# Performance work log

Hardware: AMD Instinct MI355X
Metric: run time of the kernel (lower is better)

The kernel has to match this reference:

```python
import jax, jax.numpy as jnp
import numpy as np

B, N, DIN, D, PHI, RHO, L = 4096, 10, 32, 128, 256, 128, 3
EPS = 1e-5


def setup_inputs() -> dict:
    key = jax.random.key(0)
    ks = jax.random.split(key, 24)
    def p(k, shape):
        return jax.random.normal(k, shape, jnp.float32) * 0.05
    return {
        "A": jax.random.normal(ks[0], (B, N, N), jnp.float32),
        "X": jax.random.normal(ks[1], (B, N, DIN), jnp.float32),
        "home_mask": jax.random.randint(ks[2], (B, N), 0, 2).astype(jnp.int32),
        "We1": p(ks[3], (DIN, D)), "be1": p(ks[4], (D,)),
        "We2": p(ks[5], (D, D)), "be2": p(ks[6], (D,)),
        "rgcn_w": p(ks[7], (L, 2, D, D)),      # per-relation weights
        "rgcn_root": p(ks[8], (L, D, D)),       # root (self) weight
        "rgcn_b": p(ks[9], (L, D)),
        "l1w": p(ks[10], (L, D, D)), "l1b": p(ks[11], (L, D)),
        "l2w": p(ks[12], (L, D, D)), "l2b": p(ks[13], (L, D)),
        "ln_g": jnp.ones((D,), jnp.float32), "ln_b": jnp.zeros((D,), jnp.float32),
        "p1w": p(ks[14], (D, PHI)), "p1b": p(ks[15], (PHI,)),
        "p2w": p(ks[16], (PHI, PHI)), "p2b": p(ks[17], (PHI,)),
        "r1w": p(ks[18], (PHI, RHO)), "r1b": p(ks[19], (RHO,)),
        "r2w": p(ks[20], (RHO, 1)), "r2b": p(ks[21], (1,)),
    }


def _layernorm(x, g, b):
    mu = x.mean(-1, keepdims=True)
    var = ((x - mu) ** 2).mean(-1, keepdims=True)
    return (x - mu) / jnp.sqrt(var + EPS) * g + b


def reference(A, X, home_mask, We1, be1, We2, be2, rgcn_w, rgcn_root, rgcn_b,
              l1w, l1b, l2w, l2b, ln_g, ln_b, p1w, p1b, p2w, p2b,
              r1w, r1b, r2w, r2b):
    BN = B * N
    hm = home_mask.astype(jnp.float32)
    am = 1.0 - hm
    # embedders (dropout layers are identity in eval)
    H = jax.nn.relu(X @ We1 + be1)
    H = (H @ We2 + be2).reshape(BN, D)
    # A ~ randn is nonzero everywhere -> edge list = all (b,i,j) pairs,
    # in the same row-major order torch.nonzero produces.
    bidx = jnp.repeat(jnp.arange(BN), N)          # b*N+i for each edge (row)
    row = bidx
    col = (jnp.repeat(jnp.arange(B), N * N) * N + jnp.tile(jnp.arange(N), BN))
    ew = A.reshape(-1)                             # edge weight
    aw = jnp.abs(ew)
    m1 = (ew > 0).astype(jnp.float32)              # relation 1 mask
    m0 = 1.0 - m1                                  # relation 0 mask
    agg = jnp.zeros_like(H)
    for l in range(L):
        H = H + agg
        # RGCNConv (mean aggregation per relation + root + bias)
        xj = H[row]                                # [E, D] gather of sources
        s0 = jax.ops.segment_sum(xj * m0[:, None], col, num_segments=BN)
        s1 = jax.ops.segment_sum(xj * m1[:, None], col, num_segments=BN)
        c0 = jax.ops.segment_sum(m0, col, num_segments=BN)
        c1 = jax.ops.segment_sum(m1, col, num_segments=BN)
        mean0 = s0 / jnp.maximum(c0, 1.0)[:, None]
        mean1 = s1 / jnp.maximum(c1, 1.0)[:, None]
        H2 = mean0 @ rgcn_w[l, 0] + mean1 @ rgcn_w[l, 1] + H @ rgcn_root[l] + rgcn_b[l]
        # outer gather-scale-scatter
        msg = H2[col] * aw[:, None]                # [E, D]
        agg = jax.ops.segment_sum(msg, row, num_segments=BN)
        agg = jax.nn.relu(_layernorm(agg, ln_g, ln_b))
        # Linear -> ReLU -> (Dropout=id) -> Linear
        agg = jax.nn.relu(agg @ l1w[l] + l1b[l])
        agg = agg @ l2w[l] + l2b[l]
    H = (H + agg).reshape(B, N, D)
    # DeepSet phi (dropout = identity)
    phi = jax.nn.relu(H @ p1w + p1b)
    phi = jax.nn.relu(phi @ p2w + p2b)             # [B, N, PHI]
    hs = (phi * hm[..., None]).sum(axis=1)
    aws = (phi * am[..., None]).sum(axis=1)
    def rho(s):
        return (jax.nn.relu(s @ r1w + r1b) @ r2w + r2b)[..., 0]
    return 0.5 + 0.5 * jnp.tanh(rho(hs) - rho(aws))
```

## Files before the change

### kernel.cpp

```cpp
#include <hip/hip_runtime.h>
#include <math.h>

#define B_    4096
#define N_    10
#define DIN_  32
#define D_    128
#define PHI_  256
#define RHO_  128
#define L_    3
#define EPS_  1e-5f

__device__ __forceinline__ short f2hs(float f) {
    union { _Float16 h; short s; } u;
    u.h = (_Float16)f;
    return u.s;
}
__device__ __forceinline__ float hs2f(short s) {
    union { _Float16 h; short s; } u;
    u.s = s;
    return (float)u.h;
}

typedef short   s16x8 __attribute__((ext_vector_type(8)));
typedef _Float16 h16x8 __attribute__((ext_vector_type(8)));
typedef float   f32x4 __attribute__((ext_vector_type(4)));
typedef float   v2f   __attribute__((ext_vector_type(2)));

__device__ __forceinline__ h16x8 ld8h(const short* p) {
    union { s16x8 s; h16x8 h; } u;
    u.s = *(const s16x8*)p;
    return u.h;
}

__device__ __forceinline__ v2f splat2(float s) { v2f r; r.x = s; r.y = s; return r; }
__device__ __forceinline__ v2f fma2(v2f a, v2f b, v2f c) { return __builtin_elementwise_fma(a, b, c); }

#define WS_WE1 0
#define WS_WE2 4096
#define WS_RGW 20480
#define WS_RGR 118784
#define WS_L1  167936
#define WS_L2  217088
#define WS_P1  266240
#define WS_P2  299008
#define WS_R1  364544

__global__ __launch_bounds__(64)
void prep_weights(const float* __restrict__ We1, const float* __restrict__ We2,
                  const float* __restrict__ rgw, const float* __restrict__ rgr,
                  const float* __restrict__ l1w, const float* __restrict__ l2w,
                  const float* __restrict__ p1w, const float* __restrict__ p2w,
                  const float* __restrict__ r1w, short* __restrict__ ws)
{
    int bi = blockIdx.x, l = threadIdx.x;
    const float* src; int KS, Nw, dstOff, tt;
    if      (bi <   8) { src = We1; KS = 1; Nw = 128; dstOff = WS_WE1; tt = bi; }
    else if (bi <  40) { src = We2; KS = 4; Nw = 128; dstOff = WS_WE2; tt = bi - 8; }
    else if (bi < 232) { int m = (bi - 40) >> 5;  src = rgw + m * 16384; KS = 4; Nw = 128; dstOff = WS_RGW + m * 16384; tt = (bi - 40)  & 31; }
    else if (bi < 328) { int m = (bi - 232) >> 5; src = rgr + m * 16384; KS = 4; Nw = 128; dstOff = WS_RGR + m * 16384; tt = (bi - 232) & 31; }
    else if (bi < 424) { int m = (bi - 328) >> 5; src = l1w + m * 16384; KS = 4; Nw = 128; dstOff = WS_L1  + m * 16384; tt = (bi - 328) & 31; }
    else if (bi < 520) { int m = (bi - 424) >> 5; src = l2w + m * 16384; KS = 4; Nw = 128; dstOff = WS_L2  + m * 16384; tt = (bi - 424) & 31; }
    else if (bi < 584) { src = p1w; KS = 4; Nw = 256; dstOff = WS_P1; tt = bi - 520; }
    else if (bi < 712) { src = p2w; KS = 8; Nw = 256; dstOff = WS_P2; tt = bi - 584; }
    else               { src = r1w; KS = 8; Nw = 128; dstOff = WS_R1; tt = bi - 712; }
    int nt = tt / KS, ks = tt - nt * KS;
    int kbase = ks * 32 + (l >> 4) * 8;
    int col   = nt * 16 + (l & 15);
    union { short s[8]; int4 v; } u;
#pragma unroll
    for (int j = 0; j < 8; ++j)
        u.s[j] = f2hs(src[(size_t)(kbase + j) * Nw + col]);
    *(int4*)(ws + dstOff + ((size_t)tt * 64 + l) * 8) = u.v;
}


template<int NT>
__device__ __forceinline__ void initC(f32x4* acc, const float* __restrict__ bias, int c16) {
#pragma unroll
    for (int nt = 0; nt < NT; ++nt) {
        float bv = bias[nt * 16 + c16];
        acc[nt] = (f32x4){bv, bv, bv, bv};
    }
}

template<int KS, int NT>
__device__ __forceinline__ void mm_a16(const short* __restrict__ Wf, const short* __restrict__ Ab,
                                       int ldA, int mrow, int q, int l, f32x4* acc) {
#pragma unroll
    for (int ks = 0; ks < KS; ++ks) {
        h16x8 a = ld8h(Ab + mrow * ldA + ks * 32 + q * 8);
#pragma unroll
        for (int nt = 0; nt < NT; ++nt) {
            h16x8 bv = ld8h(Wf + ((size_t)(nt * KS + ks) * 64 + l) * 8);
            acc[nt] = __builtin_amdgcn_mfma_f32_16x16x32_f16(a, bv, acc[nt], 0, 0, 0);
        }
    }
}

template<int KS, int NT>
__device__ __forceinline__ void mm_a32(const short* __restrict__ Wf, const float* __restrict__ Af,
                                       int ldA, int mrow, int q, int l, f32x4* acc) {
#pragma unroll
    for (int ks = 0; ks < KS; ++ks) {
        const float* p = Af + mrow * ldA + ks * 32 + q * 8;
        f32x4 x0 = *(const f32x4*)p;
        f32x4 x1 = *(const f32x4*)(p + 4);
        h16x8 a;
        a[0] = (_Float16)x0[0]; a[1] = (_Float16)x0[1]; a[2] = (_Float16)x0[2]; a[3] = (_Float16)x0[3];
        a[4] = (_Float16)x1[0]; a[5] = (_Float16)x1[1]; a[6] = (_Float16)x1[2]; a[7] = (_Float16)x1[3];
#pragma unroll
        for (int nt = 0; nt < NT; ++nt) {
            h16x8 bv = ld8h(Wf + ((size_t)(nt * KS + ks) * 64 + l) * 8);
            acc[nt] = __builtin_amdgcn_mfma_f32_16x16x32_f16(a, bv, acc[nt], 0, 0, 0);
        }
    }
}

template<int KS>
__device__ __forceinline__ void mm8p_a16(const short* __restrict__ Wf,
                                         const short* __restrict__ Ab, int ldA,
                                         int mrow, int q, int l, f32x4* acc)
{
    const short* ap = Ab + mrow * ldA + q * 8;
    const short* wp = Wf + l * 8;
    h16x8 acur = ld8h(ap);
    h16x8 bcur[8], bnxt[8];
#pragma unroll
    for (int nt = 0; nt < 8; ++nt) bcur[nt] = ld8h(wp + (size_t)nt * KS * 512);
#pragma unroll
    for (int ks = 0; ks < KS; ++ks) {
        h16x8 anxt = acur;
#pragma unroll
        for (int nt = 0; nt < 8; ++nt) bnxt[nt] = bcur[nt];
        if (ks + 1 < KS) {
            anxt = ld8h(ap + (ks + 1) * 32);
#pragma unroll
            for (int nt = 0; nt < 8; ++nt)
                bnxt[nt] = ld8h(wp + (size_t)(nt * KS + ks + 1) * 512);
        }
#pragma unroll
        for (int nt = 0; nt < 8; ++nt)
            acc[nt] = __builtin_amdgcn_mfma_f32_16x16x32_f16(acur, bcur[nt], acc[nt], 0, 0, 0);
        acur = anxt;
#pragma unroll
        for (int nt = 0; nt < 8; ++nt) bcur[nt] = bnxt[nt];
    }
}

template<int KS>
__device__ __forceinline__ void mm8p_a32(const short* __restrict__ Wf,
                                         const float* __restrict__ Af, int ldA,
                                         int mrow, int q, int l, f32x4* acc)
{
    const float* ap = Af + mrow * ldA + q * 8;
    const short* wp = Wf + l * 8;
    auto cvt = [&](int ks) {
        f32x4 x0 = *(const f32x4*)(ap + ks * 32);
        f32x4 x1 = *(const f32x4*)(ap + ks * 32 + 4);
        h16x8 a;
        a[0] = (_Float16)x0[0]; a[1] = (_Float16)x0[1]; a[2] = (_Float16)x0[2]; a[3] = (_Float16)x0[3];
        a[4] = (_Float16)x1[0]; a[5] = (_Float16)x1[1]; a[6] = (_Float16)x1[2]; a[7] = (_Float16)x1[3];
        return a;
    };
    h16x8 acur = cvt(0);
    h16x8 bcur[8], bnxt[8];
#pragma unroll
    for (int nt = 0; nt < 8; ++nt) bcur[nt] = ld8h(wp + (size_t)nt * KS * 512);
#pragma unroll
    for (int ks = 0; ks < KS; ++ks) {
        h16x8 anxt = acur;
#pragma unroll
        for (int nt = 0; nt < 8; ++nt) bnxt[nt] = bcur[nt];
        if (ks + 1 < KS) {
            anxt = cvt(ks + 1);
#pragma unroll
            for (int nt = 0; nt < 8; ++nt)
                bnxt[nt] = ld8h(wp + (size_t)(nt * KS + ks + 1) * 512);
        }
#pragma unroll
        for (int nt = 0; nt < 8; ++nt)
            acc[nt] = __builtin_amdgcn_mfma_f32_16x16x32_f16(acur, bcur[nt], acc[nt], 0, 0, 0);
        acur = anxt;
#pragma unroll
        for (int nt = 0; nt < 8; ++nt) bcur[nt] = bnxt[nt];
    }
}

template<int NT, bool RELU>
__device__ __forceinline__ void storeC16(const f32x4* acc, short* __restrict__ dst,
                                         int ldD, int q, int c16) {
#pragma unroll
    for (int nt = 0; nt < NT; ++nt) {
#pragma unroll
        for (int i = 0; i < 4; ++i) {
            int r = q * 4 + i;
            if (r < 10) {
                float v = acc[nt][i];
                if (RELU) v = fmaxf(v, 0.f);
                dst[r * ldD + nt * 16 + c16] = f2hs(v);
            }
        }
    }
}

#define HLD 132
#define MLD 136
#define GLD 264

__global__ __launch_bounds__(64, 2)
void gcn_main(const float* __restrict__ A, const float* __restrict__ X,
              const int* __restrict__ home_mask,
              const float* __restrict__ be1, const float* __restrict__ be2,
              const float* __restrict__ rgcn_b,
              const float* __restrict__ l1b, const float* __restrict__ l2b,
              const float* __restrict__ ln_g, const float* __restrict__ ln_b,
              const float* __restrict__ p1b, const float* __restrict__ p2b,
              const float* __restrict__ r1b, const float* __restrict__ r2w,
              const short* __restrict__ ws, float* __restrict__ out)
{
    const int b   = blockIdx.x;
    const int l   = threadIdx.x;
    const int q   = l >> 4;
    const int c16 = l & 15;
    const int mrow = (c16 < 10) ? c16 : 9;

    __shared__ __align__(16) float HfS[N_ * HLD];
    __shared__ __align__(16) short Me0S[N_ * MLD];
    __shared__ __align__(16) short Me1S[N_ * MLD];
    __shared__ __align__(16) short GbS[N_ * GLD];
    __shared__ __align__(16) short RhoS[2 * 256];
    __shared__ float AabsS[100], M1S[100];
    __shared__ float invc0S[N_], invc1S[N_];
    __shared__ float hmfS[16], awfS[16];

    {
        const float* Ab = A + (size_t)b * 100;
#pragma unroll
        for (int e = l; e < 100; e += 64) {
            float a = Ab[e];
            AabsS[e] = fabsf(a);
            M1S[e]  = (a > 0.f) ? 1.f : 0.f;
        }
        if (l < 16) {
            float hm = 0.f, aw = 0.f;
            if (l < 10) { hm = (float)home_mask[b * N_ + l]; aw = 1.f - hm; }
            hmfS[l] = hm; awfS[l] = aw;
        }
        if (l < 10) {
            float c1 = 0.f;
#pragma unroll
            for (int i = 0; i < 10; ++i) c1 += M1S[i * 10 + l];
            invc1S[l] = 1.f / fmaxf(c1, 1.f);
            invc0S[l] = 1.f / fmaxf(10.f - c1, 1.f);
        }
    }

    {
        f32x4 acc[8];
        initC<8>(acc, be1, c16);
        const float* xg = X + (size_t)b * (N_ * DIN_) + mrow * DIN_ + q * 8;
        f32x4 x0 = *(const f32x4*)xg;
        f32x4 x1 = *(const f32x4*)(xg + 4);
        h16x8 a;
        a[0] = (_Float16)x0[0]; a[1] = (_Float16)x0[1]; a[2] = (_Float16)x0[2]; a[3] = (_Float16)x0[3];
        a[4] = (_Float16)x1[0]; a[5] = (_Float16)x1[1]; a[6] = (_Float16)x1[2]; a[7] = (_Float16)x1[3];
#pragma unroll
        for (int nt = 0; nt < 8; ++nt) {
            h16x8 bv = ld8h(ws + WS_WE1 + ((size_t)nt * 64 + l) * 8);
            acc[nt] = __builtin_amdgcn_mfma_f32_16x16x32_f16(a, bv, acc[nt], 0, 0, 0);
        }
        storeC16<8, true>(acc, GbS, GLD, q, c16);
    }
    {
        f32x4 acc[8];
        initC<8>(acc, be2, c16);
        mm8p_a16<4>(ws + WS_WE2, GbS, GLD, mrow, q, l, acc);
#pragma unroll
        for (int nt = 0; nt < 8; ++nt)
#pragma unroll
            for (int i = 0; i < 4; ++i) {
                int r = q * 4 + i;
                if (r < 10) HfS[r * HLD + nt * 16 + c16] = acc[nt][i];
            }
    }

    const v2f lg2 = *(const v2f*)(ln_g + 2 * l);
    const v2f lb2 = *(const v2f*)(ln_b + 2 * l);

    for (int ll = 0; ll < L_; ++ll) {
        {
            v2f hv[N_];
#pragma unroll
            for (int i = 0; i < N_; ++i) hv[i] = *(const v2f*)(HfS + i * HLD + 2 * l);
            v2f st = hv[0];
#pragma unroll
            for (int i = 1; i < N_; ++i) st += hv[i];
#pragma unroll
            for (int j = 0; j < N_; ++j) {
                v2f s1 = splat2(0.f);
#pragma unroll
                for (int i = 0; i < N_; ++i) s1 = fma2(splat2(M1S[i * 10 + j]), hv[i], s1);
                v2f m0 = (st - s1) * splat2(invc0S[j]);
                v2f m1 = s1 * splat2(invc1S[j]);
                short2 w0; w0.x = f2hs(m0.x); w0.y = f2hs(m0.y);
                short2 w1; w1.x = f2hs(m1.x); w1.y = f2hs(m1.y);
                *(short2*)(Me0S + j * MLD + 2 * l) = w0;
                *(short2*)(Me1S + j * MLD + 2 * l) = w1;
            }
        }
        {
            f32x4 acc[8];
            initC<8>(acc, rgcn_b + ll * D_, c16);
            mm8p_a16<4>(ws + WS_RGW + (size_t)(ll * 2 + 0) * 16384, Me0S, MLD, mrow, q, l, acc);
            mm8p_a16<4>(ws + WS_RGW + (size_t)(ll * 2 + 1) * 16384, Me1S, MLD, mrow, q, l, acc);
            mm8p_a32<4>(ws + WS_RGR + (size_t)ll * 16384, HfS, HLD, mrow, q, l, acc);
            storeC16<8, false>(acc, GbS, GLD, q, c16);
        }
        {
            v2f ag[N_];
#pragma unroll
            for (int i = 0; i < N_; ++i) ag[i] = splat2(0.f);
#pragma unroll
            for (int j = 0; j < N_; ++j) {
                short2 hh = *(const short2*)(GbS + j * GLD + 2 * l);
                v2f h2; h2.x = hs2f(hh.x); h2.y = hs2f(hh.y);
#pragma unroll
                for (int i = 0; i < N_; ++i)
                    ag[i] = fma2(splat2(AabsS[i * 10 + j]), h2, ag[i]);
            }
#pragma unroll
            for (int i = 0; i < N_; ++i) {
                float s  = ag[i].x + ag[i].y;
                float ss = fmaf(ag[i].x, ag[i].x, ag[i].y * ag[i].y);
#pragma unroll
                for (int off = 32; off > 0; off >>= 1) {
                    s  += __shfl_xor(s,  off);
                    ss += __shfl_xor(ss, off);
                }
                float mu   = s * (1.f / 128.f);
                float var  = ss * (1.f / 128.f) - mu * mu;
                float rstd = rsqrtf(var + EPS_);
                v2f v = fma2((ag[i] - splat2(mu)) * splat2(rstd), lg2, lb2);
                short2 wv; wv.x = f2hs(fmaxf(v.x, 0.f)); wv.y = f2hs(fmaxf(v.y, 0.f));
                *(short2*)(GbS + i * GLD + 2 * l) = wv;
            }
        }
        {
            f32x4 acc[8];
            initC<8>(acc, l1b + ll * D_, c16);
            mm8p_a16<4>(ws + WS_L1 + (size_t)ll * 16384, GbS, GLD, mrow, q, l, acc);
            storeC16<8, true>(acc, GbS + 128, GLD, q, c16);
        }
        {
            f32x4 acc[8];
            initC<8>(acc, l2b + ll * D_, c16);
            mm8p_a16<4>(ws + WS_L2 + (size_t)ll * 16384, GbS + 128, GLD, mrow, q, l, acc);
#pragma unroll
            for (int nt = 0; nt < 8; ++nt)
#pragma unroll
                for (int i = 0; i < 4; ++i) {
                    int r = q * 4 + i;
                    if (r < 10) HfS[r * HLD + nt * 16 + c16] += acc[nt][i];
                }
        }
    }

    {
        f32x4 acc[16];
        initC<16>(acc, p1b, c16);
        mm_a32<4, 16>(ws + WS_P1, HfS, HLD, mrow, q, l, acc);
        storeC16<16, true>(acc, GbS, GLD, q, c16);
    }
    {
        f32x4 acc[16];
        initC<16>(acc, p2b, c16);
        mm_a16<8, 16>(ws + WS_P2, GbS, GLD, mrow, q, l, acc);
        float hm0 = hmfS[q * 4 + 0], hm1 = hmfS[q * 4 + 1], hm2 = hmfS[q * 4 + 2], hm3 = hmfS[q * 4 + 3];
        float aw0 = awfS[q * 4 + 0], aw1 = awfS[q * 4 + 1], aw2 = awfS[q * 4 + 2], aw3 = awfS[q * 4 + 3];
#pragma unroll
        for (int t = 0; t < 16; ++t) {
            float v0 = fmaxf(acc[t][0], 0.f), v1 = fmaxf(acc[t][1], 0.f);
            float v2 = fmaxf(acc[t][2], 0.f), v3 = fmaxf(acc[t][3], 0.f);
            float hp = hm0 * v0 + hm1 * v1 + hm2 * v2 + hm3 * v3;
            float ap = aw0 * v0 + aw1 * v1 + aw2 * v2 + aw3 * v3;
            hp += __shfl_xor(hp, 16); hp += __shfl_xor(hp, 32);
            ap += __shfl_xor(ap, 16); ap += __shfl_xor(ap, 32);
            if (l < 16) {
                RhoS[t * 16 + l]       = f2hs(hp);
                RhoS[256 + t * 16 + l] = f2hs(ap);
            }
        }
    }
    {
        f32x4 acc[8];
        initC<8>(acc, r1b, c16);
        const int rr = (c16 < 2) ? c16 : 0;
        mm_a16<8, 8>(ws + WS_R1, RhoS, 256, rr, q, l, acc);
        float d = 0.f;
        if (q == 0) {
#pragma unroll
            for (int t = 0; t < 8; ++t) {
                float vh = fmaxf(acc[t][0], 0.f);
                float va = fmaxf(acc[t][1], 0.f);
                d = fmaf(vh - va, r2w[t * 16 + c16], d);
            }
        }
#pragma unroll
        for (int off = 32; off > 0; off >>= 1) d += __shfl_xor(d, off);
        if (l == 0) out[b] = 0.5f + 0.5f * tanhf(d);
    }
}

extern "C" void kernel_launch(void* const* d_in, const int* in_sizes, int n_in,
                              void* d_out, int out_size, void* d_ws, size_t ws_size,
                              hipStream_t stream) {
    const float* A         = (const float*)d_in[0];
    const float* X         = (const float*)d_in[1];
    const int*   home_mask = (const int*)  d_in[2];
    const float* We1       = (const float*)d_in[3];
    const float* be1       = (const float*)d_in[4];
    const float* We2       = (const float*)d_in[5];
    const float* be2       = (const float*)d_in[6];
    const float* rgcn_w    = (const float*)d_in[7];
    const float* rgcn_root = (const float*)d_in[8];
    const float* rgcn_b    = (const float*)d_in[9];
    const float* l1w       = (const float*)d_in[10];
    const float* l1b       = (const float*)d_in[11];
    const float* l2w       = (const float*)d_in[12];
    const float* l2b       = (const float*)d_in[13];
    const float* ln_g      = (const float*)d_in[14];
    const float* ln_b      = (const float*)d_in[15];
    const float* p1w       = (const float*)d_in[16];
    const float* p1b       = (const float*)d_in[17];
    const float* p2w       = (const float*)d_in[18];
    const float* p2b       = (const float*)d_in[19];
    const float* r1w       = (const float*)d_in[20];
    const float* r1b       = (const float*)d_in[21];
    const float* r2w       = (const float*)d_in[22];

    short* ws = (short*)d_ws;

    prep_weights<<<776, 64, 0, stream>>>(We1, We2, rgcn_w, rgcn_root,
                                         l1w, l2w, p1w, p2w, r1w, ws);
    gcn_main<<<B_, 64, 0, stream>>>(A, X, home_mask, be1, be2, rgcn_b,
                                    l1b, l2b, ln_g, ln_b, p1b, p2b,
                                    r1b, r2w, ws, (float*)d_out);
}
```

Baseline: 263.2 us.

## Split per-graph work across four wavefronts per block with shared-memory syncs

Each block now has 256 threads instead of a single 64-lane wave. The four waves split the output columns of every matmul, and the rows of the mean-aggregation and the LayerNorm aggregation, with __syncthreads between stages. The goal is to cut per-block serial latency and raise the number of waves available to hide memory and MFMA latency. The cost is many block barriers per layer, and every wave now reads the same A operand from LDS. The software-pipelined 8-tile matmul helpers are dropped in favour of the simple loops.

```diff
diff --git a/kernel.cpp b/kernel.cpp
--- a/kernel.cpp
+++ b/kernel.cpp
@@ -21,10 +21,10 @@
     return (float)u.h;
 }
 
-typedef short   s16x8 __attribute__((ext_vector_type(8)));
+typedef short    s16x8 __attribute__((ext_vector_type(8)));
 typedef _Float16 h16x8 __attribute__((ext_vector_type(8)));
-typedef float   f32x4 __attribute__((ext_vector_type(4)));
-typedef float   v2f   __attribute__((ext_vector_type(2)));
+typedef float    f32x4 __attribute__((ext_vector_type(4)));
+typedef float    v2f   __attribute__((ext_vector_type(2)));
 
 __device__ __forceinline__ h16x8 ld8h(const short* p) {
     union { s16x8 s; h16x8 h; } u;
@@ -74,30 +74,30 @@
 }
 
 
-template<int NT>
+template<int NTP>
 __device__ __forceinline__ void initC(f32x4* acc, const float* __restrict__ bias, int c16) {
 #pragma unroll
-    for (int nt = 0; nt < NT; ++nt) {
-        float bv = bias[nt * 16 + c16];
-        acc[nt] = (f32x4){bv, bv, bv, bv};
-    }
-}
-
-template<int KS, int NT>
+    for (int j = 0; j < NTP; ++j) {
+        float bv = bias[j * 16 + c16];
+        acc[j] = (f32x4){bv, bv, bv, bv};
+    }
+}
+
+template<int KS, int NTP>
 __device__ __forceinline__ void mm_a16(const short* __restrict__ Wf, const short* __restrict__ Ab,
                                        int ldA, int mrow, int q, int l, f32x4* acc) {
 #pragma unroll
     for (int ks = 0; ks < KS; ++ks) {
         h16x8 a = ld8h(Ab + mrow * ldA + ks * 32 + q * 8);
 #pragma unroll
-        for (int nt = 0; nt < NT; ++nt) {
-            h16x8 bv = ld8h(Wf + ((size_t)(nt * KS + ks) * 64 + l) * 8);
-            acc[nt] = __builtin_amdgcn_mfma_f32_16x16x32_f16(a, bv, acc[nt], 0, 0, 0);
-        }
-    }
-}
-
-template<int KS, int NT>
+        for (int j = 0; j < NTP; ++j) {
+            h16x8 bv = ld8h(Wf + ((size_t)(j * KS + ks) * 64 + l) * 8);
+            acc[j] = __builtin_amdgcn_mfma_f32_16x16x32_f16(a, bv, acc[j], 0, 0, 0);
+        }
+    }
+}
+
+template<int KS, int NTP>
 __device__ __forceinline__ void mm_a32(const short* __restrict__ Wf, const float* __restrict__ Af,
                                        int ldA, int mrow, int q, int l, f32x4* acc) {
 #pragma unroll
@@ -109,95 +109,25 @@
         a[0] = (_Float16)x0[0]; a[1] = (_Float16)x0[1]; a[2] = (_Float16)x0[2]; a[3] = (_Float16)x0[3];
         a[4] = (_Float16)x1[0]; a[5] = (_Float16)x1[1]; a[6] = (_Float16)x1[2]; a[7] = (_Float16)x1[3];
 #pragma unroll
-        for (int nt = 0; nt < NT; ++nt) {
-            h16x8 bv = ld8h(Wf + ((size_t)(nt * KS + ks) * 64 + l) * 8);
-            acc[nt] = __builtin_amdgcn_mfma_f32_16x16x32_f16(a, bv, acc[nt], 0, 0, 0);
-        }
-    }
-}
-
-template<int KS>
-__device__ __forceinline__ void mm8p_a16(const short* __restrict__ Wf,
-                                         const short* __restrict__ Ab, int ldA,
-                                         int mrow, int q, int l, f32x4* acc)
-{
-    const short* ap = Ab + mrow * ldA + q * 8;
-    const short* wp = Wf + l * 8;
-    h16x8 acur = ld8h(ap);
-    h16x8 bcur[8], bnxt[8];
-#pragma unroll
-    for (int nt = 0; nt < 8; ++nt) bcur[nt] = ld8h(wp + (size_t)nt * KS * 512);
-#pragma unroll
-    for (int ks = 0; ks < KS; ++ks) {
-        h16x8 anxt = acur;
-#pragma unroll
-        for (int nt = 0; nt < 8; ++nt) bnxt[nt] = bcur[nt];
-        if (ks + 1 < KS) {
-            anxt = ld8h(ap + (ks + 1) * 32);
-#pragma unroll
-            for (int nt = 0; nt < 8; ++nt)
-                bnxt[nt] = ld8h(wp + (size_t)(nt * KS + ks + 1) * 512);
-        }
-#pragma unroll
-        for (int nt = 0; nt < 8; ++nt)
-            acc[nt] = __builtin_amdgcn_mfma_f32_16x16x32_f16(acur, bcur[nt], acc[nt], 0, 0, 0);
-        acur = anxt;
-#pragma unroll
-        for (int nt = 0; nt < 8; ++nt) bcur[nt] = bnxt[nt];
-    }
-}
-
-template<int KS>
-__device__ __forceinline__ void mm8p_a32(const short* __restrict__ Wf,
-                                         const float* __restrict__ Af, int ldA,
-                                         int mrow, int q, int l, f32x4* acc)
-{
-    const float* ap = Af + mrow * ldA + q * 8;
-    const short* wp = Wf + l * 8;
-    auto cvt = [&](int ks) {
-        f32x4 x0 = *(const f32x4*)(ap + ks * 32);
-        f32x4 x1 = *(const f32x4*)(ap + ks * 32 + 4);
-        h16x8 a;
-        a[0] = (_Float16)x0[0]; a[1] = (_Float16)x0[1]; a[2] = (_Float16)x0[2]; a[3] = (_Float16)x0[3];
-        a[4] = (_Float16)x1[0]; a[5] = (_Float16)x1[1]; a[6] = (_Float16)x1[2]; a[7] = (_Float16)x1[3];
-        return a;
-    };
-    h16x8 acur = cvt(0);
-    h16x8 bcur[8], bnxt[8];
-#pragma unroll
-    for (int nt = 0; nt < 8; ++nt) bcur[nt] = ld8h(wp + (size_t)nt * KS * 512);
-#pragma unroll
-    for (int ks = 0; ks < KS; ++ks) {
-        h16x8 anxt = acur;
-#pragma unroll
-        for (int nt = 0; nt < 8; ++nt) bnxt[nt] = bcur[nt];
-        if (ks + 1 < KS) {
-            anxt = cvt(ks + 1);
-#pragma unroll
-            for (int nt = 0; nt < 8; ++nt)
-                bnxt[nt] = ld8h(wp + (size_t)(nt * KS + ks + 1) * 512);
-        }
-#pragma unroll
-        for (int nt = 0; nt < 8; ++nt)
-            acc[nt] = __builtin_amdgcn_mfma_f32_16x16x32_f16(acur, bcur[nt], acc[nt], 0, 0, 0);
-        acur = anxt;
-#pragma unroll
-        for (int nt = 0; nt < 8; ++nt) bcur[nt] = bnxt[nt];
-    }
-}
-
-template<int NT, bool RELU>
+        for (int j = 0; j < NTP; ++j) {
+            h16x8 bv = ld8h(Wf + ((size_t)(j * KS + ks) * 64 + l) * 8);
+            acc[j] = __builtin_amdgcn_mfma_f32_16x16x32_f16(a, bv, acc[j], 0, 0, 0);
+        }
+    }
+}
+
+template<int NTP, bool RELU>
 __device__ __forceinline__ void storeC16(const f32x4* acc, short* __restrict__ dst,
                                          int ldD, int q, int c16) {
 #pragma unroll
-    for (int nt = 0; nt < NT; ++nt) {
+    for (int j = 0; j < NTP; ++j) {
 #pragma unroll
         for (int i = 0; i < 4; ++i) {
             int r = q * 4 + i;
             if (r < 10) {
-                float v = acc[nt][i];
+                float v = acc[j][i];
                 if (RELU) v = fmaxf(v, 0.f);
-                dst[r * ldD + nt * 16 + c16] = f2hs(v);
+                dst[r * ldD + j * 16 + c16] = f2hs(v);
             }
         }
     }
@@ -207,7 +137,7 @@
 #define MLD 136
 #define GLD 264
 
-__global__ __launch_bounds__(64, 2)
+__global__ __launch_bounds__(256, 8)
 void gcn_main(const float* __restrict__ A, const float* __restrict__ X,
               const int* __restrict__ home_mask,
               const float* __restrict__ be1, const float* __restrict__ be2,
@@ -219,7 +149,9 @@
               const short* __restrict__ ws, float* __restrict__ out)
 {
     const int b   = blockIdx.x;
-    const int l   = threadIdx.x;
+    const int tid = threadIdx.x;
+    const int wv  = tid >> 6;
+    const int l   = tid & 63;
     const int q   = l >> 4;
     const int c16 = l & 15;
     const int mrow = (c16 < 10) ? c16 : 9;
@@ -232,32 +164,21 @@
     __shared__ float AabsS[100], M1S[100];
     __shared__ float invc0S[N_], invc1S[N_];
     __shared__ float hmfS[16], awfS[16];
-
-    {
-        const float* Ab = A + (size_t)b * 100;
-#pragma unroll
-        for (int e = l; e < 100; e += 64) {
-            float a = Ab[e];
-            AabsS[e] = fabsf(a);
-            M1S[e]  = (a > 0.f) ? 1.f : 0.f;
-        }
-        if (l < 16) {
-            float hm = 0.f, aw = 0.f;
-            if (l < 10) { hm = (float)home_mask[b * N_ + l]; aw = 1.f - hm; }
-            hmfS[l] = hm; awfS[l] = aw;
-        }
-        if (l < 10) {
-            float c1 = 0.f;
-#pragma unroll
-            for (int i = 0; i < 10; ++i) c1 += M1S[i * 10 + l];
-            invc1S[l] = 1.f / fmaxf(c1, 1.f);
-            invc0S[l] = 1.f / fmaxf(10.f - c1, 1.f);
-        }
-    }
-
-    {
-        f32x4 acc[8];
-        initC<8>(acc, be1, c16);
+    __shared__ float dS[4];
+
+    if (tid < 100) {
+        float a = A[(size_t)b * 100 + tid];
+        AabsS[tid] = fabsf(a);
+        M1S[tid]  = (a > 0.f) ? 1.f : 0.f;
+    }
+    if (tid < 16) {
+        float hm = 0.f, aw = 0.f;
+        if (tid < 10) { hm = (float)home_mask[b * N_ + tid]; aw = 1.f - hm; }
+        hmfS[tid] = hm; awfS[tid] = aw;
+    }
+    {
+        f32x4 acc[2];
+        initC<2>(acc, be1 + wv * 32, c16);
         const float* xg = X + (size_t)b * (N_ * DIN_) + mrow * DIN_ + q * 8;
         f32x4 x0 = *(const f32x4*)xg;
         f32x4 x1 = *(const f32x4*)(xg + 4);
@@ -265,27 +186,35 @@
         a[0] = (_Float16)x0[0]; a[1] = (_Float16)x0[1]; a[2] = (_Float16)x0[2]; a[3] = (_Float16)x0[3];
         a[4] = (_Float16)x1[0]; a[5] = (_Float16)x1[1]; a[6] = (_Float16)x1[2]; a[7] = (_Float16)x1[3];
 #pragma unroll
-        for (int nt = 0; nt < 8; ++nt) {
-            h16x8 bv = ld8h(ws + WS_WE1 + ((size_t)nt * 64 + l) * 8);
-            acc[nt] = __builtin_amdgcn_mfma_f32_16x16x32_f16(a, bv, acc[nt], 0, 0, 0);
-        }
-        storeC16<8, true>(acc, GbS, GLD, q, c16);
-    }
-    {
-        f32x4 acc[8];
-        initC<8>(acc, be2, c16);
-        mm8p_a16<4>(ws + WS_WE2, GbS, GLD, mrow, q, l, acc);
-#pragma unroll
-        for (int nt = 0; nt < 8; ++nt)
+        for (int j = 0; j < 2; ++j) {
+            h16x8 bv = ld8h(ws + WS_WE1 + ((size_t)(wv * 2 + j) * 64 + l) * 8);
+            acc[j] = __builtin_amdgcn_mfma_f32_16x16x32_f16(a, bv, acc[j], 0, 0, 0);
+        }
+        storeC16<2, true>(acc, GbS + wv * 32, GLD, q, c16);
+    }
+    __syncthreads();
+
+    if (tid < 10) {
+        float c1 = 0.f;
+#pragma unroll
+        for (int i = 0; i < 10; ++i) c1 += M1S[i * 10 + tid];
+        invc1S[tid] = 1.f / fmaxf(c1, 1.f);
+        invc0S[tid] = 1.f / fmaxf(10.f - c1, 1.f);
+    }
+    {
+        f32x4 acc[2];
+        initC<2>(acc, be2 + wv * 32, c16);
+        mm_a16<4, 2>(ws + WS_WE2 + (size_t)wv * 4096, GbS, GLD, mrow, q, l, acc);
+        float* hb = HfS + wv * 32;
+#pragma unroll
+        for (int j = 0; j < 2; ++j)
 #pragma unroll
             for (int i = 0; i < 4; ++i) {
                 int r = q * 4 + i;
-                if (r < 10) HfS[r * HLD + nt * 16 + c16] = acc[nt][i];
-            }
-    }
-
-    const v2f lg2 = *(const v2f*)(ln_g + 2 * l);
-    const v2f lb2 = *(const v2f*)(ln_b + 2 * l);
+                if (r < 10) hb[r * HLD + j * 16 + c16] = acc[j][i];
+            }
+    }
+    __syncthreads();
 
     for (int ll = 0; ll < L_; ++ll) {
         {
@@ -295,8 +224,7 @@
             v2f st = hv[0];
 #pragma unroll
             for (int i = 1; i < N_; ++i) st += hv[i];
-#pragma unroll
-            for (int j = 0; j < N_; ++j) {
+            for (int j = wv; j < 10; j += 4) {
                 v2f s1 = splat2(0.f);
 #pragma unroll
                 for (int i = 0; i < N_; ++i) s1 = fma2(splat2(M1S[i * 10 + j]), hv[i], s1);
@@ -308,30 +236,32 @@
                 *(short2*)(Me1S + j * MLD + 2 * l) = w1;
             }
         }
-        {
-            f32x4 acc[8];
-            initC<8>(acc, rgcn_b + ll * D_, c16);
-            mm8p_a16<4>(ws + WS_RGW + (size_t)(ll * 2 + 0) * 16384, Me0S, MLD, mrow, q, l, acc);
-            mm8p_a16<4>(ws + WS_RGW + (size_t)(ll * 2 + 1) * 16384, Me1S, MLD, mrow, q, l, acc);
-            mm8p_a32<4>(ws + WS_RGR + (size_t)ll * 16384, HfS, HLD, mrow, q, l, acc);
-            storeC16<8, false>(acc, GbS, GLD, q, c16);
-        }
-        {
-            v2f ag[N_];
-#pragma unroll
-            for (int i = 0; i < N_; ++i) ag[i] = splat2(0.f);
-#pragma unroll
-            for (int j = 0; j < N_; ++j) {
-                short2 hh = *(const short2*)(GbS + j * GLD + 2 * l);
-                v2f h2; h2.x = hs2f(hh.x); h2.y = hs2f(hh.y);
-#pragma unroll
-                for (int i = 0; i < N_; ++i)
-                    ag[i] = fma2(splat2(AabsS[i * 10 + j]), h2, ag[i]);
-            }
-#pragma unroll
-            for (int i = 0; i < N_; ++i) {
-                float s  = ag[i].x + ag[i].y;
-                float ss = fmaf(ag[i].x, ag[i].x, ag[i].y * ag[i].y);
+        __syncthreads();
+        {
+            f32x4 acc[2];
+            initC<2>(acc, rgcn_b + ll * D_ + wv * 32, c16);
+            mm_a16<4, 2>(ws + WS_RGW + (size_t)(ll * 2 + 0) * 16384 + (size_t)wv * 4096, Me0S, MLD, mrow, q, l, acc);
+            mm_a16<4, 2>(ws + WS_RGW + (size_t)(ll * 2 + 1) * 16384 + (size_t)wv * 4096, Me1S, MLD, mrow, q, l, acc);
+            mm_a32<4, 2>(ws + WS_RGR + (size_t)ll * 16384 + (size_t)wv * 4096, HfS, HLD, mrow, q, l, acc);
+            storeC16<2, false>(acc, GbS + wv * 32, GLD, q, c16);
+        }
+        __syncthreads();
+        {
+            v2f lg2 = *(const v2f*)(ln_g + 2 * l);
+            v2f lb2 = *(const v2f*)(ln_b + 2 * l);
+            v2f hv2[N_];
+#pragma unroll
+            for (int jj = 0; jj < N_; ++jj) {
+                short2 hh = *(const short2*)(GbS + jj * GLD + 2 * l);
+                hv2[jj].x = hs2f(hh.x); hv2[jj].y = hs2f(hh.y);
+            }
+            for (int i = wv; i < 10; i += 4) {
+                v2f ag = splat2(0.f);
+#pragma unroll
+                for (int jj = 0; jj < N_; ++jj)
+                    ag = fma2(splat2(AabsS[i * 10 + jj]), hv2[jj], ag);
+                float s  = ag.x + ag.y;
+                float ss = fmaf(ag.x, ag.x, ag.y * ag.y);
 #pragma unroll
                 for (int off = 32; off > 0; off >>= 1) {
                     s  += __shfl_xor(s,  off);
@@ -340,45 +270,50 @@
                 float mu   = s * (1.f / 128.f);
                 float var  = ss * (1.f / 128.f) - mu * mu;
                 float rstd = rsqrtf(var + EPS_);
-                v2f v = fma2((ag[i] - splat2(mu)) * splat2(rstd), lg2, lb2);
-                short2 wv; wv.x = f2hs(fmaxf(v.x, 0.f)); wv.y = f2hs(fmaxf(v.y, 0.f));
-                *(short2*)(GbS + i * GLD + 2 * l) = wv;
-            }
-        }
-        {
-            f32x4 acc[8];
-            initC<8>(acc, l1b + ll * D_, c16);
-            mm8p_a16<4>(ws + WS_L1 + (size_t)ll * 16384, GbS, GLD, mrow, q, l, acc);
-            storeC16<8, true>(acc, GbS + 128, GLD, q, c16);
-        }
-        {
-            f32x4 acc[8];
-            initC<8>(acc, l2b + ll * D_, c16);
-            mm8p_a16<4>(ws + WS_L2 + (size_t)ll * 16384, GbS + 128, GLD, mrow, q, l, acc);
-#pragma unroll
-            for (int nt = 0; nt < 8; ++nt)
+                v2f v = fma2((ag - splat2(mu)) * splat2(rstd), lg2, lb2);
+                short2 wvv; wvv.x = f2hs(fmaxf(v.x, 0.f)); wvv.y = f2hs(fmaxf(v.y, 0.f));
+                *(short2*)(GbS + i * GLD + 128 + 2 * l) = wvv;
+            }
+        }
+        __syncthreads();
+        {
+            f32x4 acc[2];
+            initC<2>(acc, l1b + ll * D_ + wv * 32, c16);
+            mm_a16<4, 2>(ws + WS_L1 + (size_t)ll * 16384 + (size_t)wv * 4096, GbS + 128, GLD, mrow, q, l, acc);
+            storeC16<2, true>(acc, GbS + wv * 32, GLD, q, c16);
+        }
+        __syncthreads();
+        {
+            f32x4 acc[2];
+            initC<2>(acc, l2b + ll * D_ + wv * 32, c16);
+            mm_a16<4, 2>(ws + WS_L2 + (size_t)ll * 16384 + (size_t)wv * 4096, GbS, GLD, mrow, q, l, acc);
+            float* hb = HfS + wv * 32;
+#pragma unroll
+            for (int j = 0; j < 2; ++j)
 #pragma unroll
                 for (int i = 0; i < 4; ++i) {
                     int r = q * 4 + i;
-                    if (r < 10) HfS[r * HLD + nt * 16 + c16] += acc[nt][i];
+                    if (r < 10) hb[r * HLD + j * 16 + c16] += acc[j][i];
                 }
         }
-    }
-
-    {
-        f32x4 acc[16];
-        initC<16>(acc, p1b, c16);
-        mm_a32<4, 16>(ws + WS_P1, HfS, HLD, mrow, q, l, acc);
-        storeC16<16, true>(acc, GbS, GLD, q, c16);
-    }
-    {
-        f32x4 acc[16];
-        initC<16>(acc, p2b, c16);
-        mm_a16<8, 16>(ws + WS_P2, GbS, GLD, mrow, q, l, acc);
+        __syncthreads();
+    }
+
+    {
+        f32x4 acc[4];
+        initC<4>(acc, p1b + wv * 64, c16);
+        mm_a32<4, 4>(ws + WS_P1 + (size_t)wv * 8192, HfS, HLD, mrow, q, l, acc);
+        storeC16<4, true>(acc, GbS + wv * 64, GLD, q, c16);
+    }
+    __syncthreads();
+    {
+        f32x4 acc[4];
+        initC<4>(acc, p2b + wv * 64, c16);
+        mm_a16<8, 4>(ws + WS_P2 + (size_t)wv * 16384, GbS, GLD, mrow, q, l, acc);
         float hm0 = hmfS[q * 4 + 0], hm1 = hmfS[q * 4 + 1], hm2 = hmfS[q * 4 + 2], hm3 = hmfS[q * 4 + 3];
         float aw0 = awfS[q * 4 + 0], aw1 = awfS[q * 4 + 1], aw2 = awfS[q * 4 + 2], aw3 = awfS[q * 4 + 3];
 #pragma unroll
-        for (int t = 0; t < 16; ++t) {
+        for (int t = 0; t < 4; ++t) {
             float v0 = fmaxf(acc[t][0], 0.f), v1 = fmaxf(acc[t][1], 0.f);
             float v2 = fmaxf(acc[t][2], 0.f), v3 = fmaxf(acc[t][3], 0.f);
             float hp = hm0 * v0 + hm1 * v1 + hm2 * v2 + hm3 * v3;
@@ -386,29 +321,32 @@
             hp += __shfl_xor(hp, 16); hp += __shfl_xor(hp, 32);
             ap += __shfl_xor(ap, 16); ap += __shfl_xor(ap, 32);
             if (l < 16) {
-                RhoS[t * 16 + l]       = f2hs(hp);
-                RhoS[256 + t * 16 + l] = f2hs(ap);
-            }
-        }
-    }
-    {
-        f32x4 acc[8];
-        initC<8>(acc, r1b, c16);
+                RhoS[(wv * 4 + t) * 16 + l]       = f2hs(hp);
+                RhoS[256 + (wv * 4 + t) * 16 + l] = f2hs(ap);
+            }
+        }
+    }
+    __syncthreads();
+    {
+        f32x4 acc[2];
+        initC<2>(acc, r1b + wv * 32, c16);
         const int rr = (c16 < 2) ? c16 : 0;
-        mm_a16<8, 8>(ws + WS_R1, RhoS, 256, rr, q, l, acc);
+        mm_a16<8, 2>(ws + WS_R1 + (size_t)wv * 8192, RhoS, 256, rr, q, l, acc);
         float d = 0.f;
         if (q == 0) {
 #pragma unroll
-            for (int t = 0; t < 8; ++t) {
+            for (int t = 0; t < 2; ++t) {
                 float vh = fmaxf(acc[t][0], 0.f);
                 float va = fmaxf(acc[t][1], 0.f);
-                d = fmaf(vh - va, r2w[t * 16 + c16], d);
+                d = fmaf(vh - va, r2w[(wv * 2 + t) * 16 + c16], d);
             }
         }
 #pragma unroll
         for (int off = 32; off > 0; off >>= 1) d += __shfl_xor(d, off);
-        if (l == 0) out[b] = 0.5f + 0.5f * tanhf(d);
-    }
+        if (l == 0) dS[wv] = d;
+    }
+    __syncthreads();
+    if (tid == 0) out[b] = 0.5f + 0.5f * tanhf(dS[0] + dS[1] + dS[2] + dS[3]);
 }
 
 extern "C" void kernel_launch(void* const* d_in, const int* in_sizes, int n_in,
@@ -442,7 +380,7 @@
 
     prep_weights<<<776, 64, 0, stream>>>(We1, We2, rgcn_w, rgcn_root,
                                          l1w, l2w, p1w, p2w, r1w, ws);
-    gcn_main<<<B_, 64, 0, stream>>>(A, X, home_mask, be1, be2, rgcn_b,
-                                    l1b, l2b, ln_g, ln_b, p1b, p2b,
-                                    r1b, r2w, ws, (float*)d_out);
-}
+    gcn_main<<<B_, 256, 0, stream>>>(A, X, home_mask, be1, be2, rgcn_b,
+                                     l1b, l2b, ln_g, ln_b, p1b, p2b,
+                                     r1b, r2w, ws, (float*)d_out);
+}
```

New measurement: 278.5 us. 5.8% more time.
